# Kernel tuning notes

Hardware: AMD Instinct MI355X
Metric: run time of the kernel (lower is better)

Reference implementation:

```python
import jax, jax.numpy as jnp
import numpy as np

B, S, D_IN, D_A, L = 4, 4000, 1024, 512, 8921


def setup_inputs() -> dict:
    key = jax.random.key(0)
    ks = jax.random.split(key, 6)
    scale_w = 1.0 / np.sqrt(D_IN)
    scale_u = 1.0 / np.sqrt(D_A)
    return {
        "x": jax.random.normal(ks[0], (B, S, D_IN), jnp.float32),
        "W_w": jax.random.normal(ks[1], (D_A, D_IN), jnp.float32) * scale_w,
        "W_b": jax.random.normal(ks[2], (D_A,), jnp.float32) * 0.01,
        "U_w": jax.random.normal(ks[3], (L, D_A), jnp.float32) * scale_u,
        "V_w": jax.random.normal(ks[4], (L, D_A), jnp.float32) * scale_u,
        "V_b": jax.random.normal(ks[5], (L,), jnp.float32) * 0.01,
    }


def reference(x, W_w, W_b, U_w, V_w, V_b):
    # z = tanh(W x): [B, S, D_A]
    z = jnp.tanh(jnp.einsum("bsd,ad->bsa", x, W_w) + W_b)
    # label-wise attention scores over sequence: [B, L, S]
    scores = jnp.einsum("la,bsa->bls", U_w, z)
    alpha = jax.nn.softmax(scores, axis=-1)
    # per-label context vectors: [B, L, D_A]
    m = jnp.einsum("bls,bsa->bla", alpha, z)
    # per-label weighted dot-product classifier: [B, L]
    y = jnp.einsum("la,bla->bl", V_w, m) + V_b
    return (y, alpha)
```

## Files before the change

kernel.cpp:

```cpp
#include <hip/hip_runtime.h>
#include <hip/hip_bf16.h>
#include <math.h>

#define B_   4
#define S_   4000
#define DIN  1024
#define DA   512
#define L_   8921

typedef __attribute__((ext_vector_type(8))) short          short8;
typedef __attribute__((ext_vector_type(4))) float          f4;
typedef __attribute__((ext_vector_type(4))) unsigned int   u4;
typedef __attribute__((ext_vector_type(4))) unsigned short us4;

static __device__ __forceinline__ unsigned short f2b(float f) {
    unsigned int u = __float_as_uint(f);
    u += 0x7fffu + ((u >> 16) & 1u);
    return (unsigned short)(u >> 16);
}
static __device__ __forceinline__ unsigned int pack2(float lo, float hi) {
    return (unsigned int)f2b(lo) | ((unsigned int)f2b(hi) << 16);
}
static __device__ __forceinline__ float b2f(unsigned short u) {
    return __uint_as_float(((unsigned int)u) << 16);
}

__global__ __launch_bounds__(256) void k_z(const float* __restrict__ x,
                                           const float* __restrict__ Ww,
                                           const float* __restrict__ Wb,
                                           unsigned short* __restrict__ z)
{
    __shared__ unsigned short lds_a[128 * 32];
    __shared__ unsigned short lds_b[128 * 32];

    const int tid  = threadIdx.x;
    const int lane = tid & 63;
    const int w    = tid >> 6;
    const int wm   = w >> 1, wn = w & 1;
    const int q    = lane >> 4, r = lane & 15;
    const int m0   = blockIdx.x * 128;
    const int n0   = blockIdx.y * 128;

    f4 acc[4][4];
#pragma unroll
    for (int i = 0; i < 4; i++)
#pragma unroll
        for (int j = 0; j < 4; j++) { f4 zz = {0.f,0.f,0.f,0.f}; acc[i][j] = zz; }

    const int row  = tid >> 1;
    const int half = tid & 1;

    for (int kk = 0; kk < DIN; kk += 32) {
        {
            const f4* src = (const f4*)(x + (size_t)(m0 + row) * DIN + kk + half * 16);
            f4 v0 = src[0], v1 = src[1], v2 = src[2], v3 = src[3];
            u4* dst = (u4*)&lds_a[row * 32 + half * 16];
            u4 o0, o1;
            o0[0] = pack2(v0[0], v0[1]); o0[1] = pack2(v0[2], v0[3]);
            o0[2] = pack2(v1[0], v1[1]); o0[3] = pack2(v1[2], v1[3]);
            o1[0] = pack2(v2[0], v2[1]); o1[1] = pack2(v2[2], v2[3]);
            o1[2] = pack2(v3[0], v3[1]); o1[3] = pack2(v3[2], v3[3]);
            dst[0] = o0; dst[1] = o1;
        }
        {
            const f4* src = (const f4*)(Ww + (size_t)(n0 + row) * DIN + kk + half * 16);
            f4 v0 = src[0], v1 = src[1], v2 = src[2], v3 = src[3];
            u4* dst = (u4*)&lds_b[row * 32 + half * 16];
            u4 o0, o1;
            o0[0] = pack2(v0[0], v0[1]); o0[1] = pack2(v0[2], v0[3]);
            o0[2] = pack2(v1[0], v1[1]); o0[3] = pack2(v1[2], v1[3]);
            o1[0] = pack2(v2[0], v2[1]); o1[1] = pack2(v2[2], v2[3]);
            o1[2] = pack2(v3[0], v3[1]); o1[3] = pack2(v3[2], v3[3]);
            dst[0] = o0; dst[1] = o1;
        }
        __syncthreads();

        short8 af[4], bfr[4];
#pragma unroll
        for (int i = 0; i < 4; i++) {
            af[i]  = *(const short8*)&lds_a[(wm * 64 + i * 16 + r) * 32 + q * 8];
            bfr[i] = *(const short8*)&lds_b[(wn * 64 + i * 16 + r) * 32 + q * 8];
        }
#pragma unroll
        for (int i = 0; i < 4; i++)
#pragma unroll
            for (int j = 0; j < 4; j++)
                acc[i][j] = __builtin_amdgcn_mfma_f32_16x16x32_bf16(af[i], bfr[j], acc[i][j], 0, 0, 0);
        __syncthreads();
    }

#pragma unroll
    for (int i = 0; i < 4; i++) {
#pragma unroll
        for (int j = 0; j < 4; j++) {
            const int col = n0 + wn * 64 + j * 16 + r;
            const float bias = Wb[col];
#pragma unroll
            for (int e = 0; e < 4; e++) {
                const int rowg = m0 + wm * 64 + i * 16 + q * 4 + e;
                z[(size_t)rowg * DA + col] = f2b(tanhf(acc[i][j][e] + bias));
            }
        }
    }
}

__global__ __launch_bounds__(256) void k_cvt(const float* __restrict__ src,
                                             unsigned short* __restrict__ dst, int n8)
{
    const int i = blockIdx.x * 256 + threadIdx.x;
    if (i < n8) {
        const f4* s = (const f4*)src + (size_t)i * 2;
        const f4 a = s[0], b = s[1];
        u4 o;
        o[0] = pack2(a[0], a[1]); o[1] = pack2(a[2], a[3]);
        o[2] = pack2(b[0], b[1]); o[3] = pack2(b[2], b[3]);
        *((u4*)dst + i) = o;
    }
}

template<bool TB16>
__global__ __launch_bounds__(256) void k_uv(const unsigned short* __restrict__ Ubf,
                                            const unsigned short* __restrict__ Vbf,
                                            const unsigned short* __restrict__ z,
                                            float* __restrict__ scores,
                                            void* __restrict__ Tout)
{
    __shared__ unsigned short lds_u[128 * 32];
    __shared__ unsigned short lds_v[128 * 32];
    __shared__ unsigned short lds_z[128 * 32];

    const int tid  = threadIdx.x;
    const int lane = tid & 63;
    const int w    = tid >> 6;
    const int wm   = w >> 1, wn = w & 1;
    const int q    = lane >> 4, r = lane & 15;
    const int b    = blockIdx.z;
    const int m0   = blockIdx.x * 128;
    const int n0   = blockIdx.y * 128;

    f4 accU[4][4], accV[4][4];
#pragma unroll
    for (int i = 0; i < 4; i++)
#pragma unroll
        for (int j = 0; j < 4; j++) {
            f4 zz = {0.f,0.f,0.f,0.f};
            accU[i][j] = zz; accV[i][j] = zz;
        }

    const int srow = tid >> 2;
    const int sseg = tid & 3;

    for (int kk = 0; kk < DA; kk += 32) {
#pragma unroll
        for (int jj = 0; jj < 2; jj++) {
            const int rr = srow + jj * 64;
            const int gm = m0 + rr;
            const int gs = n0 + rr;
            u4 zz = {0,0,0,0};
            u4 vu = zz, vv = zz, vz = zz;
            if (gm < L_) {
                vu = *(const u4*)&Ubf[(size_t)gm * DA + kk + sseg * 8];
                vv = *(const u4*)&Vbf[(size_t)gm * DA + kk + sseg * 8];
            }
            if (gs < S_) {
                vz = *(const u4*)&z[((size_t)(b * S_ + gs)) * DA + kk + sseg * 8];
            }
            *(u4*)&lds_u[rr * 32 + sseg * 8] = vu;
            *(u4*)&lds_v[rr * 32 + sseg * 8] = vv;
            *(u4*)&lds_z[rr * 32 + sseg * 8] = vz;
        }
        __syncthreads();

        short8 fu[4], fv[4], fz[4];
#pragma unroll
        for (int i = 0; i < 4; i++) {
            fu[i] = *(const short8*)&lds_u[(wm * 64 + i * 16 + r) * 32 + q * 8];
            fv[i] = *(const short8*)&lds_v[(wm * 64 + i * 16 + r) * 32 + q * 8];
            fz[i] = *(const short8*)&lds_z[(wn * 64 + i * 16 + r) * 32 + q * 8];
        }
#pragma unroll
        for (int i = 0; i < 4; i++)
#pragma unroll
            for (int j = 0; j < 4; j++) {
                accU[i][j] = __builtin_amdgcn_mfma_f32_16x16x32_bf16(fu[i], fz[j], accU[i][j], 0, 0, 0);
                accV[i][j] = __builtin_amdgcn_mfma_f32_16x16x32_bf16(fv[i], fz[j], accV[i][j], 0, 0, 0);
            }
        __syncthreads();
    }

#pragma unroll
    for (int i = 0; i < 4; i++) {
#pragma unroll
        for (int j = 0; j < 4; j++) {
            const int colg = n0 + wn * 64 + j * 16 + r;
#pragma unroll
            for (int e = 0; e < 4; e++) {
                const int rowg = m0 + wm * 64 + i * 16 + q * 4 + e;
                if (rowg < L_ && colg < S_) {
                    const size_t idx = ((size_t)b * L_ + rowg) * S_ + colg;
                    scores[idx] = accU[i][j][e];
                    if constexpr (TB16) ((unsigned short*)Tout)[idx] = f2b(accV[i][j][e]);
                    else                ((float*)Tout)[idx]          = accV[i][j][e];
                }
            }
        }
    }
}

template<bool TB16>
__global__ __launch_bounds__(256) void k_fsy(float* __restrict__ sc,
                                             const void* __restrict__ Tin,
                                             const float* __restrict__ Vbias,
                                             float* __restrict__ y)
{
    const size_t rb = (size_t)blockIdx.x * S_;
    float* p = sc + rb;
    const int tid = threadIdx.x;

    f4 v[4];
    float mx = -3.4e38f;
#pragma unroll
    for (int j = 0; j < 4; j++) {
        const int vi = tid + j * 256;
        if (vi < S_ / 4) {
            v[j] = ((const f4*)p)[vi];
            mx = fmaxf(mx, fmaxf(fmaxf(v[j][0], v[j][1]), fmaxf(v[j][2], v[j][3])));
        }
    }
#pragma unroll
    for (int off = 32; off > 0; off >>= 1) mx = fmaxf(mx, __shfl_xor(mx, off, 64));

    __shared__ float red[12];
    if ((tid & 63) == 0) red[tid >> 6] = mx;
    __syncthreads();
    mx = fmaxf(fmaxf(red[0], red[1]), fmaxf(red[2], red[3]));

    float s = 0.f;
#pragma unroll
    for (int j = 0; j < 4; j++) {
        const int vi = tid + j * 256;
        if (vi < S_ / 4) {
#pragma unroll
            for (int c = 0; c < 4; c++) { v[j][c] = __expf(v[j][c] - mx); s += v[j][c]; }
        }
    }
#pragma unroll
    for (int off = 32; off > 0; off >>= 1) s += __shfl_xor(s, off, 64);
    if ((tid & 63) == 0) red[4 + (tid >> 6)] = s;
    __syncthreads();
    s = red[4] + red[5] + red[6] + red[7];
    const float inv = 1.f / s;

    float yp = 0.f;
#pragma unroll
    for (int j = 0; j < 4; j++) {
        const int vi = tid + j * 256;
        if (vi < S_ / 4) {
            f4 o = v[j];
            o[0] *= inv; o[1] *= inv; o[2] *= inv; o[3] *= inv;
            ((f4*)p)[vi] = o;
            if constexpr (TB16) {
                const us4 tv = ((const us4*)((const unsigned short*)Tin + rb))[vi];
                yp += o[0] * b2f(tv[0]) + o[1] * b2f(tv[1]) + o[2] * b2f(tv[2]) + o[3] * b2f(tv[3]);
            } else {
                const f4 tv = ((const f4*)((const float*)Tin + rb))[vi];
                yp += o[0] * tv[0] + o[1] * tv[1] + o[2] * tv[2] + o[3] * tv[3];
            }
        }
    }
#pragma unroll
    for (int off = 32; off > 0; off >>= 1) yp += __shfl_xor(yp, off, 64);
    if ((tid & 63) == 0) red[8 + (tid >> 6)] = yp;
    __syncthreads();
    if (tid == 0) {
        const int l = (int)(blockIdx.x % (unsigned)L_);
        y[blockIdx.x] = red[8] + red[9] + red[10] + red[11] + Vbias[l];
    }
}

__global__ __launch_bounds__(256) void k_scores(const float* __restrict__ U,
                                                const unsigned short* __restrict__ z,
                                                float* __restrict__ out)
{
    __shared__ unsigned short lds_a[128 * 32];
    __shared__ unsigned short lds_b[128 * 32];

    const int tid  = threadIdx.x;
    const int lane = tid & 63;
    const int w    = tid >> 6;
    const int wm   = w >> 1, wn = w & 1;
    const int q    = lane >> 4, r = lane & 15;
    const int b    = blockIdx.z;
    const int m0   = blockIdx.x * 128;
    const int n0   = blockIdx.y * 128;

    f4 acc[4][4];
#pragma unroll
    for (int i = 0; i < 4; i++)
#pragma unroll
        for (int j = 0; j < 4; j++) { f4 zz = {0.f,0.f,0.f,0.f}; acc[i][j] = zz; }

    const int row  = tid >> 1;
    const int half = tid & 1;
    const int brow = tid >> 2;
    const int bseg = tid & 3;

    for (int kk = 0; kk < DA; kk += 32) {
        {
            u4* dst = (u4*)&lds_a[row * 32 + half * 16];
            const int gm = m0 + row;
            if (gm < L_) {
                const f4* src = (const f4*)(U + (size_t)gm * DA + kk + half * 16);
                f4 v0 = src[0], v1 = src[1], v2 = src[2], v3 = src[3];
                u4 o0, o1;
                o0[0] = pack2(v0[0], v0[1]); o0[1] = pack2(v0[2], v0[3]);
                o0[2] = pack2(v1[0], v1[1]); o0[3] = pack2(v1[2], v1[3]);
                o1[0] = pack2(v2[0], v2[1]); o1[1] = pack2(v2[2], v2[3]);
                o1[2] = pack2(v3[0], v3[1]); o1[3] = pack2(v3[2], v3[3]);
                dst[0] = o0; dst[1] = o1;
            } else {
                u4 zz = {0,0,0,0}; dst[0] = zz; dst[1] = zz;
            }
        }
#pragma unroll
        for (int jj = 0; jj < 2; jj++) {
            const int rr = brow + jj * 64;
            const int gs = n0 + rr;
            u4* dst = (u4*)&lds_b[rr * 32 + bseg * 8];
            if (gs < S_) {
                *dst = *(const u4*)&z[((size_t)(b * S_ + gs)) * DA + kk + bseg * 8];
            } else {
                u4 zz = {0,0,0,0}; *dst = zz;
            }
        }
        __syncthreads();

        short8 af[4], bfr[4];
#pragma unroll
        for (int i = 0; i < 4; i++) {
            af[i]  = *(const short8*)&lds_a[(wm * 64 + i * 16 + r) * 32 + q * 8];
            bfr[i] = *(const short8*)&lds_b[(wn * 64 + i * 16 + r) * 32 + q * 8];
        }
#pragma unroll
        for (int i = 0; i < 4; i++)
#pragma unroll
            for (int j = 0; j < 4; j++)
                acc[i][j] = __builtin_amdgcn_mfma_f32_16x16x32_bf16(af[i], bfr[j], acc[i][j], 0, 0, 0);
        __syncthreads();
    }

#pragma unroll
    for (int i = 0; i < 4; i++) {
#pragma unroll
        for (int j = 0; j < 4; j++) {
            const int colg = n0 + wn * 64 + j * 16 + r;
#pragma unroll
            for (int e = 0; e < 4; e++) {
                const int rowg = m0 + wm * 64 + i * 16 + q * 4 + e;
                if (rowg < L_ && colg < S_)
                    out[((size_t)b * L_ + rowg) * S_ + colg] = acc[i][j][e];
            }
        }
    }
}

__global__ __launch_bounds__(256) void k_softmax(float* __restrict__ a)
{
    float* p = a + (size_t)blockIdx.x * S_;
    const int tid = threadIdx.x;

    f4 v[4];
    float mx = -3.4e38f;
#pragma unroll
    for (int j = 0; j < 4; j++) {
        const int vi = tid + j * 256;
        if (vi < S_ / 4) {
            v[j] = ((const f4*)p)[vi];
            mx = fmaxf(mx, fmaxf(fmaxf(v[j][0], v[j][1]), fmaxf(v[j][2], v[j][3])));
        }
    }
#pragma unroll
    for (int off = 32; off > 0; off >>= 1) mx = fmaxf(mx, __shfl_xor(mx, off, 64));

    __shared__ float red[8];
    if ((tid & 63) == 0) red[tid >> 6] = mx;
    __syncthreads();
    mx = fmaxf(fmaxf(red[0], red[1]), fmaxf(red[2], red[3]));

    float s = 0.f;
#pragma unroll
    for (int j = 0; j < 4; j++) {
        const int vi = tid + j * 256;
        if (vi < S_ / 4) {
#pragma unroll
            for (int c = 0; c < 4; c++) { v[j][c] = __expf(v[j][c] - mx); s += v[j][c]; }
        }
    }
#pragma unroll
    for (int off = 32; off > 0; off >>= 1) s += __shfl_xor(s, off, 64);
    if ((tid & 63) == 0) red[4 + (tid >> 6)] = s;
    __syncthreads();
    s = red[4] + red[5] + red[6] + red[7];

    const float inv = 1.f / s;
#pragma unroll
    for (int j = 0; j < 4; j++) {
        const int vi = tid + j * 256;
        if (vi < S_ / 4) {
            f4 o = v[j]; o[0] *= inv; o[1] *= inv; o[2] *= inv; o[3] *= inv;
            ((f4*)p)[vi] = o;
        }
    }
}

__global__ __launch_bounds__(256) void k_transpose(const unsigned short* __restrict__ z,
                                                   unsigned short* __restrict__ zT)
{
    __shared__ unsigned short t[32][33];
    const int b  = blockIdx.z;
    const int s0 = blockIdx.x * 32;
    const int a0 = blockIdx.y * 32;
    const int c  = threadIdx.x & 31;
    const int r4 = threadIdx.x >> 5;

#pragma unroll
    for (int i = 0; i < 4; i++) {
        const int sl = r4 * 4 + i;
        t[sl][c] = z[((size_t)(b * S_ + s0 + sl)) * DA + a0 + c];
    }
    __syncthreads();
#pragma unroll
    for (int i = 0; i < 4; i++) {
        const int al = r4 * 4 + i;
        zT[((size_t)(b * DA + a0 + al)) * S_ + s0 + c] = t[c][al];
    }
}

__global__ __launch_bounds__(256) void k_mv(const float* __restrict__ alpha,
                                            const unsigned short* __restrict__ zT,
                                            const float* __restrict__ Vw,
                                            const float* __restrict__ Vb,
                                            float* __restrict__ y)
{
    __shared__ unsigned short lds_a[64 * 32];
    __shared__ unsigned short lds_b[512 * 32];
    __shared__ float yred[64];

    const int tid  = threadIdx.x;
    const int lane = tid & 63;
    const int w    = tid >> 6;
    const int q    = lane >> 4, r = lane & 15;
    const int b    = blockIdx.y;
    const int m0   = blockIdx.x * 64;

    if (tid < 64) yred[tid] = 0.f;

    f4 acc[4][8];
#pragma unroll
    for (int i = 0; i < 4; i++)
#pragma unroll
        for (int j = 0; j < 8; j++) { f4 zz = {0.f,0.f,0.f,0.f}; acc[i][j] = zz; }

    const int arow = tid >> 2;
    const int aseg = tid & 3;

    for (int kk = 0; kk < S_; kk += 32) {
        {
            u4* dst = (u4*)&lds_a[arow * 32 + aseg * 8];
            const int gl = m0 + arow;
            if (gl < L_) {
                const f4* src = (const f4*)(alpha + ((size_t)b * L_ + gl) * S_ + kk + aseg * 8);
                f4 v0 = src[0], v1 = src[1];
                u4 o;
                o[0] = pack2(v0[0], v0[1]); o[1] = pack2(v0[2], v0[3]);
                o[2] = pack2(v1[0], v1[1]); o[3] = pack2(v1[2], v1[3]);
                *dst = o;
            } else {
                u4 zz = {0,0,0,0}; *dst = zz;
            }
        }
#pragma unroll
        for (int jj = 0; jj < 8; jj++) {
            const int rr = arow + jj * 64;
            *(u4*)&lds_b[rr * 32 + aseg * 8] =
                *(const u4*)&zT[((size_t)(b * DA + rr)) * S_ + kk + aseg * 8];
        }
        __syncthreads();

        short8 af[4], bfr[8];
#pragma unroll
        for (int i = 0; i < 4; i++)
            af[i] = *(const short8*)&lds_a[(i * 16 + r) * 32 + q * 8];
#pragma unroll
        for (int j = 0; j < 8; j++)
            bfr[j] = *(const short8*)&lds_b[(w * 128 + j * 16 + r) * 32 + q * 8];
#pragma unroll
        for (int i = 0; i < 4; i++)
#pragma unroll
            for (int j = 0; j < 8; j++)
                acc[i][j] = __builtin_amdgcn_mfma_f32_16x16x32_bf16(af[i], bfr[j], acc[i][j], 0, 0, 0);
        __syncthreads();
    }

#pragma unroll
    for (int i = 0; i < 4; i++) {
#pragma unroll
        for (int e = 0; e < 4; e++) {
            const int rowl = i * 16 + q * 4 + e;
            const int gl = m0 + rowl;
            if (gl < L_) {
                float p = 0.f;
#pragma unroll
                for (int j = 0; j < 8; j++) {
                    const int col = w * 128 + j * 16 + r;
                    p += acc[i][j][e] * Vw[(size_t)gl * DA + col];
                }
                atomicAdd(&yred[rowl], p);
            }
        }
    }
    __syncthreads();
    if (tid < 64 && (m0 + tid) < L_)
        y[b * L_ + m0 + tid] = yred[tid] + Vb[m0 + tid];
}

extern "C" void kernel_launch(void* const* d_in, const int* in_sizes, int n_in,
                              void* d_out, int out_size, void* d_ws, size_t ws_size,
                              hipStream_t stream)
{
    const float* x  = (const float*)d_in[0];
    const float* Ww = (const float*)d_in[1];
    const float* Wb = (const float*)d_in[2];
    const float* Uw = (const float*)d_in[3];
    const float* Vw = (const float*)d_in[4];
    const float* Vb = (const float*)d_in[5];

    float* y     = (float*)d_out;
    float* alpha = y + (size_t)B_ * L_;

    unsigned short* z = (unsigned short*)d_ws;
    const size_t z_bytes  = (size_t)B_ * S_ * DA * 2;
    const size_t uv_bytes = (size_t)L_ * DA * 2;
    unsigned short* Ubf = (unsigned short*)((char*)d_ws + z_bytes);
    unsigned short* Vbf = (unsigned short*)((char*)d_ws + z_bytes + uv_bytes);
    char* Tp = (char*)d_ws + z_bytes + 2 * uv_bytes;
    const size_t T_f32 = (size_t)B_ * L_ * S_ * 4;
    const size_t T_b16 = (size_t)B_ * L_ * S_ * 2;
    const size_t need_f32 = z_bytes + 2 * uv_bytes + T_f32;
    const size_t need_b16 = z_bytes + 2 * uv_bytes + T_b16;

    k_z<<<dim3(125, 4), dim3(256), 0, stream>>>(x, Ww, Wb, z);

    if (ws_size >= need_f32) {
        const int n8 = (L_ * DA) / 8;
        const int gc = (n8 + 255) / 256;
        k_cvt<<<dim3(gc), dim3(256), 0, stream>>>(Uw, Ubf, n8);
        k_cvt<<<dim3(gc), dim3(256), 0, stream>>>(Vw, Vbf, n8);
        k_uv<false><<<dim3(70, 32, B_), dim3(256), 0, stream>>>(Ubf, Vbf, z, alpha, (void*)Tp);
        k_fsy<false><<<dim3(B_ * L_), dim3(256), 0, stream>>>(alpha, (const void*)Tp, Vb, y);
    } else if (ws_size >= need_b16) {
        const int n8 = (L_ * DA) / 8;
        const int gc = (n8 + 255) / 256;
        k_cvt<<<dim3(gc), dim3(256), 0, stream>>>(Uw, Ubf, n8);
        k_cvt<<<dim3(gc), dim3(256), 0, stream>>>(Vw, Vbf, n8);
        k_uv<true><<<dim3(70, 32, B_), dim3(256), 0, stream>>>(Ubf, Vbf, z, alpha, (void*)Tp);
        k_fsy<true><<<dim3(B_ * L_), dim3(256), 0, stream>>>(alpha, (const void*)Tp, Vb, y);
    } else {
        unsigned short* zT = z + (size_t)B_ * S_ * DA;
        k_scores<<<dim3(70, 32, B_), dim3(256), 0, stream>>>(Uw, z, alpha);
        k_softmax<<<dim3(B_ * L_), dim3(256), 0, stream>>>(alpha);
        k_transpose<<<dim3(125, 16, B_), dim3(256), 0, stream>>>(z, zT);
        k_mv<<<dim3(140, B_), dim3(256), 0, stream>>>(alpha, zT, Vw, Vb, y);
    }
}
```

Measured before the change: 1.696 ms.

## Use direct global-to-LDS loads with k-major layout and XCD-aware block swizzle

Adds pre-converted bf16 copies of x and W so the z GEMM and the U/V score GEMM can use global_load_lds 16-byte loads straight into a k-major LDS layout, bypassing registers. The U/V kernel gets a flattened 1D grid whose block order is remapped so consecutive work lands on the same XCD, aiming for better L2 reuse. The z GEMM moves to 64-row tiles for more blocks, the fp32-T path is dropped in favour of always storing T in bf16, and the fused softmax kernel now prefetches T alongside the scores. The cost is an extra conversion pass over x and more workspace. Clamped row indices replace the bounds checks on loads.

```diff
diff --git a/kernel.cpp b/kernel.cpp
--- a/kernel.cpp
+++ b/kernel.cpp
@@ -23,6 +23,255 @@
 }
 static __device__ __forceinline__ float b2f(unsigned short u) {
     return __uint_as_float(((unsigned int)u) << 16);
+}
+
+static __device__ __forceinline__ void gload16(const unsigned short* g, unsigned short* l) {
+    __builtin_amdgcn_global_load_lds(
+        (const __attribute__((address_space(1))) unsigned int*)g,
+        (__attribute__((address_space(3))) unsigned int*)l, 16, 0, 0);
+}
+
+__global__ __launch_bounds__(256) void k_cvt(const float* __restrict__ src,
+                                             unsigned short* __restrict__ dst, int n8)
+{
+    const int i = blockIdx.x * 256 + threadIdx.x;
+    if (i < n8) {
+        const f4* s = (const f4*)src + (size_t)i * 2;
+        const f4 a = s[0], b = s[1];
+        u4 o;
+        o[0] = pack2(a[0], a[1]); o[1] = pack2(a[2], a[3]);
+        o[2] = pack2(b[0], b[1]); o[3] = pack2(b[2], b[3]);
+        *((u4*)dst + i) = o;
+    }
+}
+
+__global__ __launch_bounds__(256) void k_z2(const unsigned short* __restrict__ xb,
+                                            const unsigned short* __restrict__ Wbf,
+                                            const float* __restrict__ Wb,
+                                            unsigned short* __restrict__ z)
+{
+    __shared__ unsigned short lds_a[4 * 64 * 8];
+    __shared__ unsigned short lds_b[4 * 128 * 8];
+
+    const int tid  = threadIdx.x;
+    const int lane = tid & 63;
+    const int w    = tid >> 6;
+    const int wm   = w >> 1, wn = w & 1;
+    const int q    = lane >> 4, r = lane & 15;
+    const int m0   = blockIdx.x * 64;
+    const int n0   = blockIdx.y * 128;
+
+    f4 acc[2][4];
+#pragma unroll
+    for (int i = 0; i < 2; i++)
+#pragma unroll
+        for (int j = 0; j < 4; j++) { f4 zz = {0.f,0.f,0.f,0.f}; acc[i][j] = zz; }
+
+    const unsigned short* ap0 = xb  + (size_t)(m0 + lane) * DIN + w * 8;
+    const unsigned short* bp0 = Wbf + (size_t)(n0 + lane) * DIN + w * 8;
+    const unsigned short* bp1 = Wbf + (size_t)(n0 + 64 + lane) * DIN + w * 8;
+    unsigned short* la0 = &lds_a[w * 512 + lane * 8];
+    unsigned short* lb0 = &lds_b[w * 1024 + lane * 8];
+    unsigned short* lb1 = &lds_b[w * 1024 + 512 + lane * 8];
+
+    for (int kk = 0; kk < DIN; kk += 32) {
+        gload16(ap0 + kk, la0);
+        gload16(bp0 + kk, lb0);
+        gload16(bp1 + kk, lb1);
+        __syncthreads();
+
+        short8 af[2], bfr[4];
+#pragma unroll
+        for (int i = 0; i < 2; i++)
+            af[i]  = *(const short8*)&lds_a[q * 512 + (wm * 32 + i * 16 + r) * 8];
+#pragma unroll
+        for (int j = 0; j < 4; j++)
+            bfr[j] = *(const short8*)&lds_b[q * 1024 + (wn * 64 + j * 16 + r) * 8];
+#pragma unroll
+        for (int i = 0; i < 2; i++)
+#pragma unroll
+            for (int j = 0; j < 4; j++)
+                acc[i][j] = __builtin_amdgcn_mfma_f32_16x16x32_bf16(af[i], bfr[j], acc[i][j], 0, 0, 0);
+        __syncthreads();
+    }
+
+#pragma unroll
+    for (int i = 0; i < 2; i++) {
+#pragma unroll
+        for (int j = 0; j < 4; j++) {
+            const int col = n0 + wn * 64 + j * 16 + r;
+            const float bias = Wb[col];
+#pragma unroll
+            for (int e = 0; e < 4; e++) {
+                const int rowg = m0 + wm * 32 + i * 16 + q * 4 + e;
+                z[(size_t)rowg * DA + col] = f2b(tanhf(acc[i][j][e] + bias));
+            }
+        }
+    }
+}
+
+__global__ __launch_bounds__(256) void k_uv2(const unsigned short* __restrict__ Ubf,
+                                             const unsigned short* __restrict__ Vbf,
+                                             const unsigned short* __restrict__ z,
+                                             float* __restrict__ scores,
+                                             unsigned short* __restrict__ T)
+{
+    __shared__ unsigned short lds_u[4096];
+    __shared__ unsigned short lds_v[4096];
+    __shared__ unsigned short lds_z[4096];
+
+    const int tid  = threadIdx.x;
+    const int lane = tid & 63;
+    const int w    = tid >> 6;
+    const int wm   = w >> 1, wn = w & 1;
+    const int q    = lane >> 4, r = lane & 15;
+
+    const int f    = blockIdx.x;
+    const int work = (f & 7) * 1120 + (f >> 3);
+    const int mi   = work % 70;
+    const int t    = work / 70;
+    const int b    = t >> 5;
+    const int nb   = t & 31;
+    const int m0   = mi * 128;
+    const int n0   = nb * 128;
+
+    f4 accU[4][4], accV[4][4];
+#pragma unroll
+    for (int i = 0; i < 4; i++)
+#pragma unroll
+        for (int j = 0; j < 4; j++) {
+            f4 zz = {0.f,0.f,0.f,0.f};
+            accU[i][j] = zz; accV[i][j] = zz;
+        }
+
+    const int mg0 = m0 + lane,      mg1 = m0 + 64 + lane;
+    const int mr0 = mg0 < L_ ? mg0 : L_ - 1;
+    const int mr1 = mg1 < L_ ? mg1 : L_ - 1;
+    const int sg0 = n0 + lane,      sg1 = n0 + 64 + lane;
+    const int sr0 = sg0 < S_ ? sg0 : S_ - 1;
+    const int sr1 = sg1 < S_ ? sg1 : S_ - 1;
+
+    const unsigned short* up0 = Ubf + (size_t)mr0 * DA + w * 8;
+    const unsigned short* up1 = Ubf + (size_t)mr1 * DA + w * 8;
+    const unsigned short* vp0 = Vbf + (size_t)mr0 * DA + w * 8;
+    const unsigned short* vp1 = Vbf + (size_t)mr1 * DA + w * 8;
+    const unsigned short* zp0 = z + ((size_t)b * S_ + sr0) * DA + w * 8;
+    const unsigned short* zp1 = z + ((size_t)b * S_ + sr1) * DA + w * 8;
+
+    unsigned short* lu0 = &lds_u[w * 1024 + lane * 8];
+    unsigned short* lu1 = &lds_u[w * 1024 + 512 + lane * 8];
+    unsigned short* lv0 = &lds_v[w * 1024 + lane * 8];
+    unsigned short* lv1 = &lds_v[w * 1024 + 512 + lane * 8];
+    unsigned short* lz0 = &lds_z[w * 1024 + lane * 8];
+    unsigned short* lz1 = &lds_z[w * 1024 + 512 + lane * 8];
+
+    for (int kk = 0; kk < DA; kk += 32) {
+        gload16(up0 + kk, lu0); gload16(up1 + kk, lu1);
+        gload16(vp0 + kk, lv0); gload16(vp1 + kk, lv1);
+        gload16(zp0 + kk, lz0); gload16(zp1 + kk, lz1);
+        __syncthreads();
+
+        short8 fu[4], fv[4], fz[4];
+#pragma unroll
+        for (int i = 0; i < 4; i++) {
+            fu[i] = *(const short8*)&lds_u[q * 1024 + (wm * 64 + i * 16 + r) * 8];
+            fv[i] = *(const short8*)&lds_v[q * 1024 + (wm * 64 + i * 16 + r) * 8];
+            fz[i] = *(const short8*)&lds_z[q * 1024 + (wn * 64 + i * 16 + r) * 8];
+        }
+#pragma unroll
+        for (int i = 0; i < 4; i++)
+#pragma unroll
+            for (int j = 0; j < 4; j++) {
+                accU[i][j] = __builtin_amdgcn_mfma_f32_16x16x32_bf16(fu[i], fz[j], accU[i][j], 0, 0, 0);
+                accV[i][j] = __builtin_amdgcn_mfma_f32_16x16x32_bf16(fv[i], fz[j], accV[i][j], 0, 0, 0);
+            }
+        __syncthreads();
+    }
+
+#pragma unroll
+    for (int i = 0; i < 4; i++) {
+#pragma unroll
+        for (int j = 0; j < 4; j++) {
+            const int colg = n0 + wn * 64 + j * 16 + r;
+#pragma unroll
+            for (int e = 0; e < 4; e++) {
+                const int rowg = m0 + wm * 64 + i * 16 + q * 4 + e;
+                if (rowg < L_ && colg < S_) {
+                    const size_t idx = ((size_t)b * L_ + rowg) * S_ + colg;
+                    scores[idx] = accU[i][j][e];
+                    T[idx]      = f2b(accV[i][j][e]);
+                }
+            }
+        }
+    }
+}
+
+__global__ __launch_bounds__(256) void k_fsy2(float* __restrict__ sc,
+                                              const unsigned short* __restrict__ T,
+                                              const float* __restrict__ Vbias,
+                                              float* __restrict__ y)
+{
+    const size_t rb = (size_t)blockIdx.x * S_;
+    float* p = sc + rb;
+    const unsigned short* tp = T + rb;
+    const int tid = threadIdx.x;
+
+    f4 v[4];
+    us4 tv[4];
+    float mx = -3.4e38f;
+#pragma unroll
+    for (int j = 0; j < 4; j++) {
+        const int vi = tid + j * 256;
+        if (vi < S_ / 4) {
+            v[j]  = ((const f4*)p)[vi];
+            tv[j] = ((const us4*)tp)[vi];
+            mx = fmaxf(mx, fmaxf(fmaxf(v[j][0], v[j][1]), fmaxf(v[j][2], v[j][3])));
+        }
+    }
+#pragma unroll
+    for (int off = 32; off > 0; off >>= 1) mx = fmaxf(mx, __shfl_xor(mx, off, 64));
+
+    __shared__ float red[12];
+    if ((tid & 63) == 0) red[tid >> 6] = mx;
+    __syncthreads();
+    mx = fmaxf(fmaxf(red[0], red[1]), fmaxf(red[2], red[3]));
+
+    float s = 0.f;
+#pragma unroll
+    for (int j = 0; j < 4; j++) {
+        const int vi = tid + j * 256;
+        if (vi < S_ / 4) {
+#pragma unroll
+            for (int c = 0; c < 4; c++) { v[j][c] = __expf(v[j][c] - mx); s += v[j][c]; }
+        }
+    }
+#pragma unroll
+    for (int off = 32; off > 0; off >>= 1) s += __shfl_xor(s, off, 64);
+    if ((tid & 63) == 0) red[4 + (tid >> 6)] = s;
+    __syncthreads();
+    s = red[4] + red[5] + red[6] + red[7];
+    const float inv = 1.f / s;
+
+    float yp = 0.f;
+#pragma unroll
+    for (int j = 0; j < 4; j++) {
+        const int vi = tid + j * 256;
+        if (vi < S_ / 4) {
+            f4 o = v[j];
+            o[0] *= inv; o[1] *= inv; o[2] *= inv; o[3] *= inv;
+            ((f4*)p)[vi] = o;
+            yp += o[0] * b2f(tv[j][0]) + o[1] * b2f(tv[j][1])
+                + o[2] * b2f(tv[j][2]) + o[3] * b2f(tv[j][3]);
+        }
+    }
+#pragma unroll
+    for (int off = 32; off > 0; off >>= 1) yp += __shfl_xor(yp, off, 64);
+    if ((tid & 63) == 0) red[8 + (tid >> 6)] = yp;
+    __syncthreads();
+    if (tid == 0) {
+        const int l = (int)(blockIdx.x % (unsigned)L_);
+        y[blockIdx.x] = red[8] + red[9] + red[10] + red[11] + Vbias[l];
+    }
 }
 
 __global__ __launch_bounds__(256) void k_z(const float* __restrict__ x,
@@ -101,180 +350,6 @@
                 z[(size_t)rowg * DA + col] = f2b(tanhf(acc[i][j][e] + bias));
             }
         }
-    }
-}
-
-__global__ __launch_bounds__(256) void k_cvt(const float* __restrict__ src,
-                                             unsigned short* __restrict__ dst, int n8)
-{
-    const int i = blockIdx.x * 256 + threadIdx.x;
-    if (i < n8) {
-        const f4* s = (const f4*)src + (size_t)i * 2;
-        const f4 a = s[0], b = s[1];
-        u4 o;
-        o[0] = pack2(a[0], a[1]); o[1] = pack2(a[2], a[3]);
-        o[2] = pack2(b[0], b[1]); o[3] = pack2(b[2], b[3]);
-        *((u4*)dst + i) = o;
-    }
-}
-
-template<bool TB16>
-__global__ __launch_bounds__(256) void k_uv(const unsigned short* __restrict__ Ubf,
-                                            const unsigned short* __restrict__ Vbf,
-                                            const unsigned short* __restrict__ z,
-                                            float* __restrict__ scores,
-                                            void* __restrict__ Tout)
-{
-    __shared__ unsigned short lds_u[128 * 32];
-    __shared__ unsigned short lds_v[128 * 32];
-    __shared__ unsigned short lds_z[128 * 32];
-
-    const int tid  = threadIdx.x;
-    const int lane = tid & 63;
-    const int w    = tid >> 6;
-    const int wm   = w >> 1, wn = w & 1;
-    const int q    = lane >> 4, r = lane & 15;
-    const int b    = blockIdx.z;
-    const int m0   = blockIdx.x * 128;
-    const int n0   = blockIdx.y * 128;
-
-    f4 accU[4][4], accV[4][4];
-#pragma unroll
-    for (int i = 0; i < 4; i++)
-#pragma unroll
-        for (int j = 0; j < 4; j++) {
-            f4 zz = {0.f,0.f,0.f,0.f};
-            accU[i][j] = zz; accV[i][j] = zz;
-        }
-
-    const int srow = tid >> 2;
-    const int sseg = tid & 3;
-
-    for (int kk = 0; kk < DA; kk += 32) {
-#pragma unroll
-        for (int jj = 0; jj < 2; jj++) {
-            const int rr = srow + jj * 64;
-            const int gm = m0 + rr;
-            const int gs = n0 + rr;
-            u4 zz = {0,0,0,0};
-            u4 vu = zz, vv = zz, vz = zz;
-            if (gm < L_) {
-                vu = *(const u4*)&Ubf[(size_t)gm * DA + kk + sseg * 8];
-                vv = *(const u4*)&Vbf[(size_t)gm * DA + kk + sseg * 8];
-            }
-            if (gs < S_) {
-                vz = *(const u4*)&z[((size_t)(b * S_ + gs)) * DA + kk + sseg * 8];
-            }
-            *(u4*)&lds_u[rr * 32 + sseg * 8] = vu;
-            *(u4*)&lds_v[rr * 32 + sseg * 8] = vv;
-            *(u4*)&lds_z[rr * 32 + sseg * 8] = vz;
-        }
-        __syncthreads();
-
-        short8 fu[4], fv[4], fz[4];
-#pragma unroll
-        for (int i = 0; i < 4; i++) {
-            fu[i] = *(const short8*)&lds_u[(wm * 64 + i * 16 + r) * 32 + q * 8];
-            fv[i] = *(const short8*)&lds_v[(wm * 64 + i * 16 + r) * 32 + q * 8];
-            fz[i] = *(const short8*)&lds_z[(wn * 64 + i * 16 + r) * 32 + q * 8];
-        }
-#pragma unroll
-        for (int i = 0; i < 4; i++)
-#pragma unroll
-            for (int j = 0; j < 4; j++) {
-                accU[i][j] = __builtin_amdgcn_mfma_f32_16x16x32_bf16(fu[i], fz[j], accU[i][j], 0, 0, 0);
-                accV[i][j] = __builtin_amdgcn_mfma_f32_16x16x32_bf16(fv[i], fz[j], accV[i][j], 0, 0, 0);
-            }
-        __syncthreads();
-    }
-
-#pragma unroll
-    for (int i = 0; i < 4; i++) {
-#pragma unroll
-        for (int j = 0; j < 4; j++) {
-            const int colg = n0 + wn * 64 + j * 16 + r;
-#pragma unroll
-            for (int e = 0; e < 4; e++) {
-                const int rowg = m0 + wm * 64 + i * 16 + q * 4 + e;
-                if (rowg < L_ && colg < S_) {
-                    const size_t idx = ((size_t)b * L_ + rowg) * S_ + colg;
-                    scores[idx] = accU[i][j][e];
-                    if constexpr (TB16) ((unsigned short*)Tout)[idx] = f2b(accV[i][j][e]);
-                    else                ((float*)Tout)[idx]          = accV[i][j][e];
-                }
-            }
-        }
-    }
-}
-
-template<bool TB16>
-__global__ __launch_bounds__(256) void k_fsy(float* __restrict__ sc,
-                                             const void* __restrict__ Tin,
-                                             const float* __restrict__ Vbias,
-                                             float* __restrict__ y)
-{
-    const size_t rb = (size_t)blockIdx.x * S_;
-    float* p = sc + rb;
-    const int tid = threadIdx.x;
-
-    f4 v[4];
-    float mx = -3.4e38f;
-#pragma unroll
-    for (int j = 0; j < 4; j++) {
-        const int vi = tid + j * 256;
-        if (vi < S_ / 4) {
-            v[j] = ((const f4*)p)[vi];
-            mx = fmaxf(mx, fmaxf(fmaxf(v[j][0], v[j][1]), fmaxf(v[j][2], v[j][3])));
-        }
-    }
-#pragma unroll
-    for (int off = 32; off > 0; off >>= 1) mx = fmaxf(mx, __shfl_xor(mx, off, 64));
-
-    __shared__ float red[12];
-    if ((tid & 63) == 0) red[tid >> 6] = mx;
-    __syncthreads();
-    mx = fmaxf(fmaxf(red[0], red[1]), fmaxf(red[2], red[3]));
-
-    float s = 0.f;
-#pragma unroll
-    for (int j = 0; j < 4; j++) {
-        const int vi = tid + j * 256;
-        if (vi < S_ / 4) {
-#pragma unroll
-            for (int c = 0; c < 4; c++) { v[j][c] = __expf(v[j][c] - mx); s += v[j][c]; }
-        }
-    }
-#pragma unroll
-    for (int off = 32; off > 0; off >>= 1) s += __shfl_xor(s, off, 64);
-    if ((tid & 63) == 0) red[4 + (tid >> 6)] = s;
-    __syncthreads();
-    s = red[4] + red[5] + red[6] + red[7];
-    const float inv = 1.f / s;
-
-    float yp = 0.f;
-#pragma unroll
-    for (int j = 0; j < 4; j++) {
-        const int vi = tid + j * 256;
-        if (vi < S_ / 4) {
-            f4 o = v[j];
-            o[0] *= inv; o[1] *= inv; o[2] *= inv; o[3] *= inv;
-            ((f4*)p)[vi] = o;
-            if constexpr (TB16) {
-                const us4 tv = ((const us4*)((const unsigned short*)Tin + rb))[vi];
-                yp += o[0] * b2f(tv[0]) + o[1] * b2f(tv[1]) + o[2] * b2f(tv[2]) + o[3] * b2f(tv[3]);
-            } else {
-                const f4 tv = ((const f4*)((const float*)Tin + rb))[vi];
-                yp += o[0] * tv[0] + o[1] * tv[1] + o[2] * tv[2] + o[3] * tv[3];
-            }
-        }
-    }
-#pragma unroll
-    for (int off = 32; off > 0; off >>= 1) yp += __shfl_xor(yp, off, 64);
-    if ((tid & 63) == 0) red[8 + (tid >> 6)] = yp;
-    __syncthreads();
-    if (tid == 0) {
-        const int l = (int)(blockIdx.x % (unsigned)L_);
-        y[blockIdx.x] = red[8] + red[9] + red[10] + red[11] + Vbias[l];
     }
 }
 
@@ -538,35 +613,34 @@
     float* y     = (float*)d_out;
     float* alpha = y + (size_t)B_ * L_;
 
-    unsigned short* z = (unsigned short*)d_ws;
     const size_t z_bytes  = (size_t)B_ * S_ * DA * 2;
+    const size_t xb_bytes = (size_t)B_ * S_ * DIN * 2;
+    const size_t wb_bytes = (size_t)DA * DIN * 2;
     const size_t uv_bytes = (size_t)L_ * DA * 2;
-    unsigned short* Ubf = (unsigned short*)((char*)d_ws + z_bytes);
-    unsigned short* Vbf = (unsigned short*)((char*)d_ws + z_bytes + uv_bytes);
-    char* Tp = (char*)d_ws + z_bytes + 2 * uv_bytes;
-    const size_t T_f32 = (size_t)B_ * L_ * S_ * 4;
-    const size_t T_b16 = (size_t)B_ * L_ * S_ * 2;
-    const size_t need_f32 = z_bytes + 2 * uv_bytes + T_f32;
-    const size_t need_b16 = z_bytes + 2 * uv_bytes + T_b16;
-
-    k_z<<<dim3(125, 4), dim3(256), 0, stream>>>(x, Ww, Wb, z);
-
-    if (ws_size >= need_f32) {
-        const int n8 = (L_ * DA) / 8;
-        const int gc = (n8 + 255) / 256;
-        k_cvt<<<dim3(gc), dim3(256), 0, stream>>>(Uw, Ubf, n8);
-        k_cvt<<<dim3(gc), dim3(256), 0, stream>>>(Vw, Vbf, n8);
-        k_uv<false><<<dim3(70, 32, B_), dim3(256), 0, stream>>>(Ubf, Vbf, z, alpha, (void*)Tp);
-        k_fsy<false><<<dim3(B_ * L_), dim3(256), 0, stream>>>(alpha, (const void*)Tp, Vb, y);
-    } else if (ws_size >= need_b16) {
-        const int n8 = (L_ * DA) / 8;
-        const int gc = (n8 + 255) / 256;
-        k_cvt<<<dim3(gc), dim3(256), 0, stream>>>(Uw, Ubf, n8);
-        k_cvt<<<dim3(gc), dim3(256), 0, stream>>>(Vw, Vbf, n8);
-        k_uv<true><<<dim3(70, 32, B_), dim3(256), 0, stream>>>(Ubf, Vbf, z, alpha, (void*)Tp);
-        k_fsy<true><<<dim3(B_ * L_), dim3(256), 0, stream>>>(alpha, (const void*)Tp, Vb, y);
+    const size_t T_bytes  = (size_t)B_ * L_ * S_ * 2;
+    const size_t need     = z_bytes + xb_bytes + wb_bytes + 2 * uv_bytes + T_bytes;
+
+    unsigned short* z   = (unsigned short*)d_ws;
+    unsigned short* xb  = (unsigned short*)((char*)d_ws + z_bytes);
+    unsigned short* Wbf = (unsigned short*)((char*)d_ws + z_bytes + xb_bytes);
+    unsigned short* Ubf = (unsigned short*)((char*)d_ws + z_bytes + xb_bytes + wb_bytes);
+    unsigned short* Vbf = (unsigned short*)((char*)d_ws + z_bytes + xb_bytes + wb_bytes + uv_bytes);
+    unsigned short* T   = (unsigned short*)((char*)d_ws + z_bytes + xb_bytes + wb_bytes + 2 * uv_bytes);
+
+    if (ws_size >= need) {
+        const int n8x = (B_ * S_ * DIN) / 8;
+        const int n8w = (DA * DIN) / 8;
+        const int n8u = (L_ * DA) / 8;
+        k_cvt<<<dim3((n8x + 255) / 256), dim3(256), 0, stream>>>(x,  xb,  n8x);
+        k_cvt<<<dim3((n8w + 255) / 256), dim3(256), 0, stream>>>(Ww, Wbf, n8w);
+        k_cvt<<<dim3((n8u + 255) / 256), dim3(256), 0, stream>>>(Uw, Ubf, n8u);
+        k_cvt<<<dim3((n8u + 255) / 256), dim3(256), 0, stream>>>(Vw, Vbf, n8u);
+        k_z2<<<dim3(250, 4), dim3(256), 0, stream>>>(xb, Wbf, Wb, z);
+        k_uv2<<<dim3(8960), dim3(256), 0, stream>>>(Ubf, Vbf, z, alpha, T);
+        k_fsy2<<<dim3(B_ * L_), dim3(256), 0, stream>>>(alpha, T, Vb, y);
     } else {
         unsigned short* zT = z + (size_t)B_ * S_ * DA;
+        k_z<<<dim3(125, 4), dim3(256), 0, stream>>>(x, Ww, Wb, z);
         k_scores<<<dim3(70, 32, B_), dim3(256), 0, stream>>>(Uw, z, alpha);
         k_softmax<<<dim3(B_ * L_), dim3(256), 0, stream>>>(alpha);
         k_transpose<<<dim3(125, 16, B_), dim3(256), 0, stream>>>(z, zT);
```

After: 1.904 ms. +12.3%, slower.
